# Kernel optimization log

Hardware: AMD Instinct MI355X
Metric: run time of the kernel (lower is better)

The kernel has to match this reference:

```python
import jax, jax.numpy as jnp
import numpy as np

K = 7        # neighborhood kernel size
HEADS = 4


def _layernorm(x, g, b, eps=1e-5):
    m = x.mean(-1, keepdims=True)
    v = x.var(-1, keepdims=True)
    return (x - m) * jax.lax.rsqrt(v + eps) * g + b


def _neigh_idx(n, k):
    # NATTEN semantics: window of size k centered on the query, shifted to stay in-bounds.
    starts = np.clip(np.arange(n) - k // 2, 0, n - k)
    idx = starts[:, None] + np.arange(k)                 # (n, k) absolute neighbor coords
    rel = idx - np.arange(n)[:, None] + (k - 1)          # (n, k) in [0, 2k-2] -> rpb index
    return jnp.asarray(idx), jnp.asarray(rel)


def _na2d(x, qkv_w, qkv_b, rpb, proj_w, proj_b, k=K, heads=HEADS):
    # x: (B, H, W, C) neighborhood attention (NATTEN NeighborhoodAttention2D)
    B, H, W, C = x.shape
    dh = C // heads
    qkv = (x @ qkv_w + qkv_b).reshape(B, H, W, 3, heads, dh)
    q = qkv[..., 0, :, :] * (dh ** -0.5)                 # (B,H,W,n,d)
    kk = qkv[..., 1, :, :]
    v = qkv[..., 2, :, :]
    ih, rh = _neigh_idx(H, k)
    iw, rw = _neigh_idx(W, k)
    kg = kk[:, ih][:, :, :, iw]                          # (B,H,k,W,k,n,d)
    vg = v[:, ih][:, :, :, iw]
    logits = jnp.einsum('bhwnd,bhiwjnd->bnhwij', q, kg)  # (B,n,H,W,k,k)
    bias = rpb[:, rh][:, :, :, rw]                       # (n,H,k,W,k)
    bias = jnp.transpose(bias, (0, 1, 3, 2, 4))          # (n,H,W,k,k)
    logits = logits + bias[None]
    attn = jax.nn.softmax(logits.reshape(B, heads, H, W, k * k), axis=-1)
    attn = attn.reshape(B, heads, H, W, k, k)
    out = jnp.einsum('bnhwij,bhiwjnd->bhwnd', attn, vg).reshape(B, H, W, C)
    return out @ proj_w + proj_b


def _mixffn(x, fc1_w, fc1_b, dw_w, dw_b, fc2_w, fc2_b, b, t, H, W):
    # PosFeedForward3d: fc1 -> depthwise Conv3d(3x3x3) over (T,H,W) -> GELU -> fc2
    h = x @ fc1_w + fc1_b                                # (b*t, H*W, M)
    M = h.shape[-1]
    h = h.reshape(b, t, H, W, M)
    h = jax.lax.conv_general_dilated(
        h, dw_w, window_strides=(1, 1, 1), padding='SAME',
        dimension_numbers=('NDHWC', 'DHWIO', 'NDHWC'), feature_group_count=M) + dw_b
    h = jax.nn.gelu(h, approximate=False)
    h = h.reshape(b * t, H * W, M)
    return h @ fc2_w + fc2_b


def setup_inputs() -> dict:
    key = jax.random.key(0)
    B, C, T, H, W = 2, 128, 8, 40, 40
    L, M, k, n = 2, 512, K, HEADS
    ks = jax.random.split(key, 12)
    s = 0.02
    return {
        'x': jax.random.normal(ks[0], (B, C, T, H, W), jnp.float32),
        'ln1_g': jnp.ones((L, C)), 'ln1_b': jnp.zeros((L, C)),
        'qkv_w': jax.random.normal(ks[1], (L, C, 3 * C), jnp.float32) * s,
        'qkv_b': jnp.zeros((L, 3 * C)),
        'rpb': jax.random.normal(ks[2], (L, n, 2 * k - 1, 2 * k - 1), jnp.float32) * s,
        'proj_w': jax.random.normal(ks[3], (L, C, C), jnp.float32) * s,
        'proj_b': jnp.zeros((L, C)),
        'ln2_g': jnp.ones((L, C)), 'ln2_b': jnp.zeros((L, C)),
        'fc1_w': jax.random.normal(ks[4], (L, C, M), jnp.float32) * s,
        'fc1_b': jnp.zeros((L, M)),
        'dw_w': jax.random.normal(ks[5], (L, 3, 3, 3, 1, M), jnp.float32) * s,
        'dw_b': jnp.zeros((L, M)),
        'fc2_w': jax.random.normal(ks[6], (L, M, C), jnp.float32) * s,
        'fc2_b': jnp.zeros((L, C)),
        'out_g': jnp.ones((C,)), 'out_b': jnp.zeros((C,)),
    }


def reference(x, ln1_g, ln1_b, qkv_w, qkv_b, rpb, proj_w, proj_b,
              ln2_g, ln2_b, fc1_w, fc1_b, dw_w, dw_b, fc2_w, fc2_b, out_g, out_b):
    b, c, t, H, W = x.shape
    h = jnp.transpose(x, (0, 2, 3, 4, 1)).reshape(b * t, H, W, c)
    L = qkv_w.shape[0]
    for i in range(L):
        h = _na2d(_layernorm(h, ln1_g[i], ln1_b[i]), qkv_w[i], qkv_b[i], rpb[i], proj_w[i], proj_b[i]) + h
        h2 = h.reshape(b * t, H * W, c)
        h2 = _mixffn(_layernorm(h2, ln2_g[i], ln2_b[i]), fc1_w[i], fc1_b[i], dw_w[i], dw_b[i], fc2_w[i], fc2_b[i], b, t, H, W) + h2
        h = h2.reshape(b * t, H, W, c)
    h = _layernorm(h, out_g, out_b)
    return jnp.transpose(h.reshape(b, t, H, W, c), (0, 4, 1, 2, 3))
```

## Files before the change

### kernel.cpp

```cpp
#include <hip/hip_runtime.h>
#include <hip/hip_bf16.h>
#include <math.h>

typedef __hip_bfloat16 bf16;
typedef __attribute__((ext_vector_type(8))) short short8;
typedef __attribute__((ext_vector_type(4))) float floatx4;
typedef __attribute__((ext_vector_type(2))) float f32x2;
typedef _Float16 h2 __attribute__((ext_vector_type(2)));
typedef __fp16 hraw2 __attribute__((ext_vector_type(2)));

static __device__ __forceinline__ h2 cvt2h(float a, float b) {
    union { hraw2 r; h2 h; } u;
    u.r = __builtin_amdgcn_cvt_pkrtz(a, b);
    return u.h;
}

#define HH 40
#define WW 40
#define CC 128
#define TT 8
#define NIMG 16
#define NTOK 25600
#define MDIM 512
#define NHEAD 4
#define KVP 1608
#define VP  1280
#define LGS 60

#define WT_QKV 0
#define WT_PROJ 49152
#define WT_FC1  65536
#define WT_FC2  131072
#define WT_L    196608

__global__ __launch_bounds__(256) void k_transpose_in(const float* __restrict__ x,
                                                      float* __restrict__ h) {
    int blk = blockIdx.x;
    int n = blk / 200; int r = blk % 200; int ci = r / 50, ri = r % 50;
    int b = n >> 3, t = n & 7;
    int c0 = ci * 32, r0 = ri * 32;
    __shared__ float tile[32][33];
    int tid = threadIdx.x;
    int lc = tid >> 5, lr = tid & 31;
    #pragma unroll
    for (int it = 0; it < 4; ++it) {
        int cc = it * 8 + lc;
        tile[cc][lr] = x[((size_t)((b * 128 + c0 + cc) * 8 + t)) * 1600 + r0 + lr];
    }
    __syncthreads();
    #pragma unroll
    for (int it = 0; it < 4; ++it) {
        int rr = it * 8 + lc;
        h[((size_t)(n * 1600 + r0 + rr)) * 128 + c0 + lr] = tile[lr][rr];
    }
}

__global__ __launch_bounds__(256) void k_wt(const float* __restrict__ qkv_w,
                                            const float* __restrict__ proj_w,
                                            const float* __restrict__ fc1_w,
                                            const float* __restrict__ fc2_w,
                                            bf16* __restrict__ wt) {
    __shared__ float tile[64][65];
    int id = blockIdx.x;
    int l = id / 48, r = id % 48;
    const float* src; bf16* dst; int K_, N_, t;
    if (r < 12)      { src = qkv_w  + l * 128 * 384; dst = wt + l * WT_L + WT_QKV; K_ = 128; N_ = 384; t = r; }
    else if (r < 16) { src = proj_w + l * 128 * 128; dst = wt + l * WT_L + WT_PROJ; K_ = 128; N_ = 128; t = r - 12; }
    else if (r < 32) { src = fc1_w  + l * 128 * 512; dst = wt + l * WT_L + WT_FC1; K_ = 128; N_ = 512; t = r - 16; }
    else             { src = fc2_w  + l * 512 * 128; dst = wt + l * WT_L + WT_FC2; K_ = 512; N_ = 128; t = r - 32; }
    int KT = K_ >> 6;
    int k0 = (t % KT) * 64, n0 = (t / KT) * 64;
    int tid = threadIdx.x;
    for (int c = tid; c < 4096; c += 256) {
        int kk = c >> 6, nn = c & 63;
        tile[kk][nn] = src[(size_t)(k0 + kk) * N_ + n0 + nn];
    }
    __syncthreads();
    for (int c = tid; c < 4096; c += 256) {
        int nn = c >> 6, kk = c & 63;
        dst[(size_t)(n0 + nn) * K_ + k0 + kk] = __float2bfloat16(tile[kk][nn]);
    }
}

template<typename OutT>
__global__ __launch_bounds__(256) void k_lngemm(const float* __restrict__ A,
                                                const bf16* __restrict__ Bt,
                                                const float* __restrict__ g,
                                                const float* __restrict__ be,
                                                const float* __restrict__ bias,
                                                OutT* __restrict__ D,
                                                int N) {
    constexpr int LDK = 40;
    __shared__ bf16 As[64 * LDK];
    __shared__ bf16 Bs[128 * LDK];
    __shared__ float sMean[64], sRstd[64], sG[128], sB[128];
    int tid = threadIdx.x;
    int m0 = blockIdx.y * 64, n0 = blockIdx.x * 128;
    {
        int row = tid >> 2, q4 = tid & 3;
        const float* p = A + (size_t)(m0 + row) * 128 + q4 * 32;
        float s = 0.f, q = 0.f;
        #pragma unroll
        for (int i = 0; i < 32; i += 4) {
            float4 f = *(const float4*)(p + i);
            s += f.x + f.y + f.z + f.w;
            q += f.x * f.x + f.y * f.y + f.z * f.z + f.w * f.w;
        }
        s += __shfl_xor(s, 1); q += __shfl_xor(q, 1);
        s += __shfl_xor(s, 2); q += __shfl_xor(q, 2);
        if (q4 == 0) {
            float mean = s * (1.0f / 128.0f);
            float var = q * (1.0f / 128.0f) - mean * mean;
            sMean[row] = mean;
            sRstd[row] = rsqrtf(var + 1e-5f);
        }
        if (tid < 128) { sG[tid] = g[tid]; sB[tid] = be[tid]; }
    }
    __syncthreads();
    int wave = tid >> 6, lane = tid & 63;
    int l15 = lane & 15, quad = lane >> 4;
    int wr = wave >> 1, wc = wave & 1;
    floatx4 acc[2][4];
    #pragma unroll
    for (int i = 0; i < 2; ++i)
        #pragma unroll
        for (int j = 0; j < 4; ++j)
            acc[i][j] = (floatx4){0.f, 0.f, 0.f, 0.f};

    for (int k0 = 0; k0 < 128; k0 += 32) {
        #pragma unroll
        for (int it = 0; it < 2; ++it) {
            int c = tid + it * 256;
            int row = c >> 3, kq = (c & 7) * 4;
            float4 f = *(const float4*)(A + (size_t)(m0 + row) * 128 + k0 + kq);
            float mean = sMean[row], rst = sRstd[row];
            float r0v = (f.x - mean) * rst * sG[k0 + kq]     + sB[k0 + kq];
            float r1v = (f.y - mean) * rst * sG[k0 + kq + 1] + sB[k0 + kq + 1];
            float r2v = (f.z - mean) * rst * sG[k0 + kq + 2] + sB[k0 + kq + 2];
            float r3v = (f.w - mean) * rst * sG[k0 + kq + 3] + sB[k0 + kq + 3];
            __hip_bfloat162 p0, p1;
            p0.x = __float2bfloat16(r0v); p0.y = __float2bfloat16(r1v);
            p1.x = __float2bfloat16(r2v); p1.y = __float2bfloat16(r3v);
            *(__hip_bfloat162*)&As[row * LDK + kq]     = p0;
            *(__hip_bfloat162*)&As[row * LDK + kq + 2] = p1;
        }
        #pragma unroll
        for (int c = tid; c < 512; c += 256) {
            int row = c >> 2, off = (c & 3) * 8;
            *(uint4*)&Bs[row * LDK + off] =
                *(const uint4*)&Bt[(size_t)(n0 + row) * 128 + k0 + off];
        }
        __syncthreads();
        short8 af[2], bfr[4];
        #pragma unroll
        for (int i = 0; i < 2; ++i)
            af[i] = *(const short8*)&As[(wr * 32 + i * 16 + l15) * LDK + quad * 8];
        #pragma unroll
        for (int j = 0; j < 4; ++j)
            bfr[j] = *(const short8*)&Bs[(wc * 64 + j * 16 + l15) * LDK + quad * 8];
        #pragma unroll
        for (int i = 0; i < 2; ++i)
            #pragma unroll
            for (int j = 0; j < 4; ++j)
                acc[i][j] = __builtin_amdgcn_mfma_f32_16x16x32_bf16(af[i], bfr[j], acc[i][j], 0, 0, 0);
        __syncthreads();
    }
    #pragma unroll
    for (int i = 0; i < 2; ++i) {
        #pragma unroll
        for (int j = 0; j < 4; ++j) {
            int nn = n0 + wc * 64 + j * 16 + l15;
            float bv = bias[nn];
            #pragma unroll
            for (int rg = 0; rg < 4; ++rg) {
                int m = m0 + wr * 32 + i * 16 + quad * 4 + rg;
                float v = acc[i][j][rg] + bv;
                if constexpr (sizeof(OutT) == 2)
                    D[(size_t)m * N + nn] = __float2bfloat16(v);
                else
                    D[(size_t)m * N + nn] = v;
            }
        }
    }
}

template<int BM, int BN, int WM, int WN, typename OutT>
__global__ __launch_bounds__(256) void k_gemm_mfma(const bf16* __restrict__ A,
                                                   const bf16* __restrict__ Bt,
                                                   const float* __restrict__ bias,
                                                   const float* __restrict__ R,
                                                   OutT* __restrict__ D,
                                                   int K, int N) {
    constexpr int LDK = 40;
    __shared__ bf16 As[BM * LDK];
    __shared__ bf16 Bs[BN * LDK];
    int tid = threadIdx.x;
    int wave = tid >> 6, lane = tid & 63;
    int l15 = lane & 15, quad = lane >> 4;
    constexpr int WCOLS = BN / WN;
    int wr = wave / WCOLS, wc = wave % WCOLS;
    int m0 = blockIdx.y * BM, n0 = blockIdx.x * BN;
    constexpr int MI = WM / 16, NJ = WN / 16;
    floatx4 acc[MI][NJ];
    #pragma unroll
    for (int i = 0; i < MI; ++i)
        #pragma unroll
        for (int j = 0; j < NJ; ++j)
            acc[i][j] = (floatx4){0.f, 0.f, 0.f, 0.f};

    for (int k0 = 0; k0 < K; k0 += 32) {
        #pragma unroll
        for (int c = tid; c < BM * 4; c += 256) {
            int row = c >> 2, off = (c & 3) * 8;
            *(uint4*)&As[row * LDK + off] =
                *(const uint4*)&A[(size_t)(m0 + row) * K + k0 + off];
        }
        #pragma unroll
        for (int c = tid; c < BN * 4; c += 256) {
            int row = c >> 2, off = (c & 3) * 8;
            *(uint4*)&Bs[row * LDK + off] =
                *(const uint4*)&Bt[(size_t)(n0 + row) * K + k0 + off];
        }
        __syncthreads();
        short8 af[MI], bfr[NJ];
        #pragma unroll
        for (int i = 0; i < MI; ++i)
            af[i] = *(const short8*)&As[(wr * WM + i * 16 + l15) * LDK + quad * 8];
        #pragma unroll
        for (int j = 0; j < NJ; ++j)
            bfr[j] = *(const short8*)&Bs[(wc * WN + j * 16 + l15) * LDK + quad * 8];
        #pragma unroll
        for (int i = 0; i < MI; ++i)
            #pragma unroll
            for (int j = 0; j < NJ; ++j)
                acc[i][j] = __builtin_amdgcn_mfma_f32_16x16x32_bf16(af[i], bfr[j], acc[i][j], 0, 0, 0);
        __syncthreads();
    }
    #pragma unroll
    for (int i = 0; i < MI; ++i) {
        #pragma unroll
        for (int j = 0; j < NJ; ++j) {
            int nn = n0 + wc * WN + j * 16 + l15;
            float bv = bias[nn];
            #pragma unroll
            for (int rg = 0; rg < 4; ++rg) {
                int m = m0 + wr * WM + i * 16 + quad * 4 + rg;
                float v = acc[i][j][rg] + bv;
                if (R) v += R[(size_t)m * N + nn];
                if constexpr (sizeof(OutT) == 2)
                    D[(size_t)m * N + nn] = __float2bfloat16(v);
                else
                    D[(size_t)m * N + nn] = v;
            }
        }
    }
}

__global__ __launch_bounds__(256) void k_gemm_ln(const bf16* __restrict__ A,
                                                 const bf16* __restrict__ Bt,
                                                 const float* __restrict__ bias,
                                                 const float* __restrict__ R,
                                                 const float* __restrict__ g,
                                                 const float* __restrict__ be,
                                                 float* __restrict__ Dres,
                                                 bf16* __restrict__ Aout,
                                                 int K) {
    constexpr int LDK = 40;
    __shared__ bf16 As[32 * LDK];
    __shared__ bf16 Bs[128 * LDK];
    __shared__ float pSum[2][32], pSq[2][32];
    __shared__ float sG[128], sB[128];
    int tid = threadIdx.x;
    int wave = tid >> 6, lane = tid & 63;
    int l15 = lane & 15, quad = lane >> 4;
    int wr = wave >> 1, wc = wave & 1;
    int m0 = blockIdx.x * 32;
    if (tid < 128) { sG[tid] = g[tid]; sB[tid] = be[tid]; }
    floatx4 acc[4];
    #pragma unroll
    for (int j = 0; j < 4; ++j) acc[j] = (floatx4){0.f, 0.f, 0.f, 0.f};

    for (int k0 = 0; k0 < K; k0 += 32) {
        if (tid < 128) {
            int row = tid >> 2, off = (tid & 3) * 8;
            *(uint4*)&As[row * LDK + off] =
                *(const uint4*)&A[(size_t)(m0 + row) * K + k0 + off];
        }
        #pragma unroll
        for (int c = tid; c < 512; c += 256) {
            int row = c >> 2, off = (c & 3) * 8;
            *(uint4*)&Bs[row * LDK + off] =
                *(const uint4*)&Bt[(size_t)row * K + k0 + off];
        }
        __syncthreads();
        short8 af = *(const short8*)&As[(wr * 16 + l15) * LDK + quad * 8];
        short8 bfr[4];
        #pragma unroll
        for (int j = 0; j < 4; ++j)
            bfr[j] = *(const short8*)&Bs[(wc * 64 + j * 16 + l15) * LDK + quad * 8];
        #pragma unroll
        for (int j = 0; j < 4; ++j)
            acc[j] = __builtin_amdgcn_mfma_f32_16x16x32_bf16(af, bfr[j], acc[j], 0, 0, 0);
        __syncthreads();
    }
    float v[4][4];
    float s[4] = {0.f, 0.f, 0.f, 0.f};
    float q[4] = {0.f, 0.f, 0.f, 0.f};
    #pragma unroll
    for (int j = 0; j < 4; ++j) {
        int nn = wc * 64 + j * 16 + l15;
        float bv = bias[nn];
        #pragma unroll
        for (int rg = 0; rg < 4; ++rg) {
            int m = wr * 16 + quad * 4 + rg;
            float val = acc[j][rg] + bv + R[(size_t)(m0 + m) * 128 + nn];
            v[j][rg] = val;
            s[rg] += val; q[rg] += val * val;
        }
    }
    #pragma unroll
    for (int o = 8; o > 0; o >>= 1) {
        #pragma unroll
        for (int rg = 0; rg < 4; ++rg) {
            s[rg] += __shfl_xor(s[rg], o);
            q[rg] += __shfl_xor(q[rg], o);
        }
    }
    if (l15 == 0) {
        #pragma unroll
        for (int rg = 0; rg < 4; ++rg) {
            int row = wr * 16 + quad * 4 + rg;
            pSum[wc][row] = s[rg];
            pSq[wc][row]  = q[rg];
        }
    }
    __syncthreads();
    #pragma unroll
    for (int rg = 0; rg < 4; ++rg) {
        int row = wr * 16 + quad * 4 + rg;
        float tot = pSum[0][row] + pSum[1][row];
        float tq  = pSq[0][row]  + pSq[1][row];
        float mean = tot * (1.0f / 128.0f);
        float var = tq * (1.0f / 128.0f) - mean * mean;
        float rst = rsqrtf(var + 1e-5f);
        size_t rb = (size_t)(m0 + row) * 128;
        #pragma unroll
        for (int j = 0; j < 4; ++j) {
            int nn = wc * 64 + j * 16 + l15;
            Dres[rb + nn] = v[j][rg];
            Aout[rb + nn] = __float2bfloat16((v[j][rg] - mean) * rst * sG[nn] + sB[nn]);
        }
    }
}

__global__ __launch_bounds__(256) void k_gemm_lnout(const bf16* __restrict__ A,
                                                    const bf16* __restrict__ Bt,
                                                    const float* __restrict__ bias,
                                                    const float* __restrict__ R,
                                                    const float* __restrict__ g,
                                                    const float* __restrict__ be,
                                                    float* __restrict__ out,
                                                    int K) {
    constexpr int LDK = 40;
    __shared__ bf16 As[32 * LDK];
    __shared__ bf16 Bs[128 * LDK];
    __shared__ float ot[32][133];
    __shared__ float sG[128], sB[128];
    int tid = threadIdx.x;
    int wave = tid >> 6, lane = tid & 63;
    int l15 = lane & 15, quad = lane >> 4;
    int wr = wave >> 1, wc = wave & 1;
    int m0 = blockIdx.x * 32;
    if (tid < 128) { sG[tid] = g[tid]; sB[tid] = be[tid]; }
    floatx4 acc[4];
    #pragma unroll
    for (int j = 0; j < 4; ++j) acc[j] = (floatx4){0.f, 0.f, 0.f, 0.f};

    for (int k0 = 0; k0 < K; k0 += 32) {
        if (tid < 128) {
            int row = tid >> 2, off = (tid & 3) * 8;
            *(uint4*)&As[row * LDK + off] =
                *(const uint4*)&A[(size_t)(m0 + row) * K + k0 + off];
        }
        #pragma unroll
        for (int c = tid; c < 512; c += 256) {
            int row = c >> 2, off = (c & 3) * 8;
            *(uint4*)&Bs[row * LDK + off] =
                *(const uint4*)&Bt[(size_t)row * K + k0 + off];
        }
        __syncthreads();
        short8 af = *(const short8*)&As[(wr * 16 + l15) * LDK + quad * 8];
        short8 bfr[4];
        #pragma unroll
        for (int j = 0; j < 4; ++j)
            bfr[j] = *(const short8*)&Bs[(wc * 64 + j * 16 + l15) * LDK + quad * 8];
        #pragma unroll
        for (int j = 0; j < 4; ++j)
            acc[j] = __builtin_amdgcn_mfma_f32_16x16x32_bf16(af, bfr[j], acc[j], 0, 0, 0);
        __syncthreads();
    }
    #pragma unroll
    for (int j = 0; j < 4; ++j) {
        int nn = wc * 64 + j * 16 + l15;
        float bv = bias[nn];
        #pragma unroll
        for (int rg = 0; rg < 4; ++rg) {
            int m = wr * 16 + quad * 4 + rg;
            ot[m][nn] = acc[j][rg] + bv + R[(size_t)(m0 + m) * 128 + nn];
        }
    }
    __syncthreads();
    int row = tid >> 3, sub = tid & 7;
    float vv[16];
    float s = 0.f, q = 0.f;
    #pragma unroll
    for (int i = 0; i < 16; ++i) {
        float v = ot[row][sub * 16 + i];
        vv[i] = v; s += v; q += v * v;
    }
    #pragma unroll
    for (int o = 4; o > 0; o >>= 1) { s += __shfl_xor(s, o); q += __shfl_xor(q, o); }
    float mean = s * (1.0f / 128.0f);
    float var = q * (1.0f / 128.0f) - mean * mean;
    float rst = rsqrtf(var + 1e-5f);
    #pragma unroll
    for (int i = 0; i < 16; ++i) {
        int ch = sub * 16 + i;
        ot[row][ch] = (vv[i] - mean) * rst * sG[ch] + sB[ch];
    }
    __syncthreads();
    int n = m0 / 1600, rem0 = m0 % 1600;
    int b = n >> 3, t = n & 7;
    #pragma unroll
    for (int it = 0; it < 16; ++it) {
        int idx = it * 256 + tid;
        int ch = idx >> 5, tk = idx & 31;
        out[((size_t)((b * 128 + ch) * 8 + t)) * 1600 + rem0 + tk] = ot[tk][ch];
    }
}

__global__ __launch_bounds__(256) void k_attn(const bf16* __restrict__ qkv,
                                              const float* __restrict__ rpb,
                                              bf16* __restrict__ out) {
    int raw = blockIdx.x;
    int blk = (raw & 7) * 320 + (raw >> 3);
    int head = blk & 3;
    int ny = blk >> 2;
    int n = ny / 40, y = ny % 40;
    int sy = min(max(y - 3, 0), HH - 7);
    __shared__ __align__(16) short KVs[7 * KVP];
    __shared__ __align__(16) float lg[40][LGS];
    int tid = threadIdx.x;
    for (int i2 = tid; i2 < 1120; i2 += 256) {
        int d8 = i2 & 3, kx = (i2 >> 2) % 40, ky = i2 / 160;
        size_t base = ((size_t)(n * 1600 + (sy + ky) * 40 + kx)) * 384 + 128 + head * 32 + d8 * 8;
        union { uint4 u; __hip_bfloat162 b[4]; } U;
        U.u = *(const uint4*)(qkv + base);
        union { short8 s; h2 h[4]; } W;
        #pragma unroll
        for (int c = 0; c < 4; ++c) {
            float2 f = __bfloat1622float2(U.b[c]);
            W.h[c] = cvt2h(f.x, f.y);
        }
        *(short8*)&KVs[ky * KVP + kx * 40 + d8 * 8] = W.s;
    }
    __syncthreads();
    for (int p2 = tid; p2 < 280; p2 += 256) {
        int xq = p2 / 7, ky = p2 - (p2 / 7) * 7;
        int sx = min(max(xq - 3, 0), WW - 7);
        const bf16* qg = qkv + ((size_t)(n * 1600 + y * 40 + xq)) * 384 + head * 32;
        union { uint4 u; __hip_bfloat162 b[4]; } U[4];
        #pragma unroll
        for (int u = 0; u < 4; ++u) U[u].u = *(const uint4*)(qg + u * 8);
        h2 qh[16];
        #pragma unroll
        for (int c = 0; c < 16; ++c) {
            float2 f = __bfloat1622float2(U[c >> 2].b[c & 3]);
            qh[c] = cvt2h(f.x, f.y);
        }
        const float* rb = rpb + head * 169 + (sy + ky - y + 6) * 13 + (sx - xq + 6);
        int kbase = ky * KVP + sx * 40;
        #pragma unroll
        for (int jx = 0; jx < 7; ++jx) {
            const h2* kp = (const h2*)&KVs[kbase + jx * 40];
            float dot = 0.f;
            #pragma unroll
            for (int c = 0; c < 16; ++c)
                dot = __builtin_amdgcn_fdot2(qh[c], kp[c], dot, false);
            lg[xq][ky * 8 + jx] = dot * 0.1767766952966369f + rb[jx];
        }
        lg[xq][ky * 8 + 7] = -1e30f;
    }
    __syncthreads();
    for (int i2 = tid; i2 < 1120; i2 += 256) {
        int d8 = i2 & 3, kx = (i2 >> 2) % 40, ky = i2 / 160;
        size_t base = ((size_t)(n * 1600 + (sy + ky) * 40 + kx)) * 384 + 256 + head * 32 + d8 * 8;
        *(uint4*)&KVs[ky * VP + kx * 32 + d8 * 8] = *(const uint4*)(qkv + base);
    }
    if (tid < 160) {
        int row = tid >> 2, q = tid & 3;
        int nb = (q == 3) ? 2 : 4;
        const float4* lp = (const float4*)&lg[row][q * 16];
        float4 f[4];
        #pragma unroll
        for (int i = 0; i < 4; ++i)
            if (i < nb) f[i] = lp[i];
        float m = -1e30f;
        #pragma unroll
        for (int i = 0; i < 4; ++i)
            if (i < nb) m = fmaxf(m, fmaxf(fmaxf(f[i].x, f[i].y), fmaxf(f[i].z, f[i].w)));
        m = fmaxf(m, __shfl_xor(m, 1));
        m = fmaxf(m, __shfl_xor(m, 2));
        float s = 0.f;
        #pragma unroll
        for (int i = 0; i < 4; ++i)
            if (i < nb) {
                f[i].x = expf(f[i].x - m); f[i].y = expf(f[i].y - m);
                f[i].z = expf(f[i].z - m); f[i].w = expf(f[i].w - m);
                s += f[i].x + f[i].y + f[i].z + f[i].w;
            }
        s += __shfl_xor(s, 1);
        s += __shfl_xor(s, 2);
        float inv = 1.0f / s;
        float4* sp = (float4*)&lg[row][q * 16];
        #pragma unroll
        for (int i = 0; i < 4; ++i)
            if (i < nb) {
                f[i].x *= inv; f[i].y *= inv; f[i].z *= inv; f[i].w *= inv;
                sp[i] = f[i];
            }
    }
    __syncthreads();
    for (int o = tid; o < 320; o += 256) {
        int xq = o >> 3, cq = o & 7;
        int sx = min(max(xq - 3, 0), WW - 7);
        float a0 = 0.f, a1 = 0.f, a2 = 0.f, a3 = 0.f;
        #pragma unroll
        for (int ky = 0; ky < 7; ++ky) {
            float4 pa = *(const float4*)&lg[xq][ky * 8];
            float4 pb = *(const float4*)&lg[xq][ky * 8 + 4];
            float ps[8] = {pa.x, pa.y, pa.z, pa.w, pb.x, pb.y, pb.z, pb.w};
            int vb = ky * VP + sx * 32 + cq * 4;
            #pragma unroll
            for (int jx = 0; jx < 7; ++jx) {
                float p = ps[jx];
                uint2 vv = *(const uint2*)&KVs[vb + jx * 32];
                float2 v0 = __bfloat1622float2(*(const __hip_bfloat162*)&vv.x);
                float2 v1 = __bfloat1622float2(*(const __hip_bfloat162*)&vv.y);
                a0 += p * v0.x; a1 += p * v0.y;
                a2 += p * v1.x; a3 += p * v1.y;
            }
        }
        __hip_bfloat162 o01, o23;
        o01.x = __float2bfloat16(a0); o01.y = __float2bfloat16(a1);
        o23.x = __float2bfloat16(a2); o23.y = __float2bfloat16(a3);
        bf16* op = out + ((size_t)(n * 1600 + y * 40 + xq)) * 128 + head * 32 + cq * 4;
        *(__hip_bfloat162*)op = o01;
        *(__hip_bfloat162*)(op + 2) = o23;
    }
}

template<int X0>
__device__ __forceinline__ void dw_body(const float* __restrict__ inp,
                                        const int* roff, const float* wr,
                                        float bs, int m, size_t outbase,
                                        bf16* __restrict__ outp) {
    float c0[9], c1[9], c2[9];
    #pragma unroll
    for (int p = 0; p < 9; ++p) {
        c0[p] = (X0 > 0) ? inp[roff[p] + (X0 - 1) * 512 + m] : 0.f;
        c1[p] = inp[roff[p] + X0 * 512 + m];
        c2[p] = inp[roff[p] + (X0 + 1) * 512 + m];
    }
    #pragma unroll
    for (int xi = 0; xi < 20; ++xi) {
        constexpr int XN_BASE = X0 + 2;
        int x = X0 + xi;
        float cn[9];
        if (XN_BASE + xi < 40) {
            #pragma unroll
            for (int p = 0; p < 9; ++p)
                cn[p] = inp[roff[p] + (XN_BASE + xi) * 512 + m];
        } else {
            #pragma unroll
            for (int p = 0; p < 9; ++p) cn[p] = 0.f;
        }
        float acc = bs;
        #pragma unroll
        for (int p = 0; p < 9; ++p)
            acc += wr[p * 3 + 0] * c0[p] + wr[p * 3 + 1] * c1[p] + wr[p * 3 + 2] * c2[p];
        float g = 0.5f * acc * (1.0f + erff(acc * 0.70710678118654752f));
        outp[outbase + (size_t)x * 512] = __float2bfloat16(g);
        #pragma unroll
        for (int p = 0; p < 9; ++p) { c0[p] = c1[p]; c1[p] = c2[p]; c2[p] = cn[p]; }
    }
}

__global__ __launch_bounds__(512, 4) void k_dwconv(const float* __restrict__ inp,
                                                   const float* __restrict__ w,
                                                   const float* __restrict__ bias,
                                                   bf16* __restrict__ outp) {
    int raw = blockIdx.x;
    int blk = (raw & 7) * 160 + (raw >> 3);
    int xh = blk & 1;
    int ny = blk >> 1;
    int n = ny / 40, y = ny - n * 40;
    int b = n >> 3, t = n & 7;
    int m = threadIdx.x;
    float wr[27];
    int roff[9];
    #pragma unroll
    for (int dt = 0; dt < 3; ++dt) {
        #pragma unroll
        for (int dy = 0; dy < 3; ++dy) {
            int p = dt * 3 + dy;
            int tt = t + dt - 1, yy = y + dy - 1;
            bool v = (tt >= 0 && tt < 8 && yy >= 0 && yy < 40);
            int tc = min(max(tt, 0), 7), yc = min(max(yy, 0), 39);
            roff[p] = ((b * 8 + tc) * 1600 + yc * 40) * 512;
            #pragma unroll
            for (int q = 0; q < 3; ++q)
                wr[p * 3 + q] = v ? w[(p * 3 + q) * 512 + m] : 0.f;
        }
    }
    float bs = bias[m];
    size_t outbase = ((size_t)(n * 1600 + y * 40)) * 512 + m;
    if (xh == 0)
        dw_body<0>(inp, roff, wr, bs, m, outbase, outp);
    else
        dw_body<20>(inp, roff, wr, bs, m, outbase, outp);
}

extern "C" void kernel_launch(void* const* d_in, const int* in_sizes, int n_in,
                              void* d_out, int out_size, void* d_ws, size_t ws_size,
                              hipStream_t stream) {
    const float* x      = (const float*)d_in[0];
    const float* ln1_g  = (const float*)d_in[1];
    const float* ln1_b  = (const float*)d_in[2];
    const float* qkv_w  = (const float*)d_in[3];
    const float* qkv_b  = (const float*)d_in[4];
    const float* rpb    = (const float*)d_in[5];
    const float* proj_w = (const float*)d_in[6];
    const float* proj_b = (const float*)d_in[7];
    const float* ln2_g  = (const float*)d_in[8];
    const float* ln2_b  = (const float*)d_in[9];
    const float* fc1_w  = (const float*)d_in[10];
    const float* fc1_b  = (const float*)d_in[11];
    const float* dw_w   = (const float*)d_in[12];
    const float* dw_b   = (const float*)d_in[13];
    const float* fc2_w  = (const float*)d_in[14];
    const float* fc2_b  = (const float*)d_in[15];
    const float* out_g  = (const float*)d_in[16];
    const float* out_b  = (const float*)d_in[17];
    float* out = (float*)d_out;

    float* h     = (float*)d_ws;
    float* f1    = h + (size_t)NTOK * 128;
    bf16* qkvb   = (bf16*)(f1 + (size_t)NTOK * 512);
    bf16* f2b    = qkvb + (size_t)NTOK * 384;
    bf16* abufA  = f2b  + (size_t)NTOK * 512;
    bf16* abufL  = abufA + (size_t)NTOK * 128;
    bf16* wt     = abufL + (size_t)NTOK * 128;

    k_wt<<<96, 256, 0, stream>>>(qkv_w, proj_w, fc1_w, fc2_w, wt);
    k_transpose_in<<<NIMG * 200, 256, 0, stream>>>(x, h);
    for (int l = 0; l < 2; ++l) {
        const bf16* wtl = wt + (size_t)l * WT_L;
        if (l == 0) {
            k_lngemm<bf16><<<dim3(3, 400), 256, 0, stream>>>(
                h, wtl + WT_QKV, ln1_g, ln1_b, qkv_b, qkvb, 384);
        } else {
            k_gemm_mfma<64, 128, 32, 64, bf16><<<dim3(3, 400), 256, 0, stream>>>(
                abufL, wtl + WT_QKV, qkv_b + 384, nullptr, qkvb, 128, 384);
        }
        k_attn<<<NIMG * HH * NHEAD, 256, 0, stream>>>(qkvb, rpb + l * 4 * 169, abufA);
        k_gemm_ln<<<800, 256, 0, stream>>>(
            abufA, wtl + WT_PROJ, proj_b + l * 128, h,
            ln2_g + l * 128, ln2_b + l * 128, h, abufL, 128);
        k_gemm_mfma<64, 128, 32, 64, float><<<dim3(4, 400), 256, 0, stream>>>(
            abufL, wtl + WT_FC1, fc1_b + l * 512, nullptr, f1, 128, 512);
        k_dwconv<<<NIMG * HH * 2, 512, 0, stream>>>(f1, dw_w + l * 27 * 512, dw_b + l * 512, f2b);
        if (l == 0) {
            k_gemm_ln<<<800, 256, 0, stream>>>(
                f2b, wtl + WT_FC2, fc2_b, h,
                ln1_g + 128, ln1_b + 128, h, abufL, 512);
        } else {
            k_gemm_lnout<<<800, 256, 0, stream>>>(
                f2b, wtl + WT_FC2, fc2_b + 128, h, out_g, out_b, out, 512);
        }
    }
}
```

Baseline: 365.1 us.

## Store fc1 output in bf16, merge prep kernels, widen attention blocks to 320 threads

```diff
diff --git a/kernel.cpp b/kernel.cpp
--- a/kernel.cpp
+++ b/kernel.cpp
@@ -33,52 +33,51 @@
 #define WT_FC2  131072
 #define WT_L    196608
 
-__global__ __launch_bounds__(256) void k_transpose_in(const float* __restrict__ x,
-                                                      float* __restrict__ h) {
-    int blk = blockIdx.x;
-    int n = blk / 200; int r = blk % 200; int ci = r / 50, ri = r % 50;
-    int b = n >> 3, t = n & 7;
-    int c0 = ci * 32, r0 = ri * 32;
-    __shared__ float tile[32][33];
+__global__ __launch_bounds__(256) void k_prep(const float* __restrict__ x,
+                                              const float* __restrict__ qkv_w,
+                                              const float* __restrict__ proj_w,
+                                              const float* __restrict__ fc1_w,
+                                              const float* __restrict__ fc2_w,
+                                              float* __restrict__ h,
+                                              bf16* __restrict__ wt) {
+    __shared__ float tileU[64 * 65];
     int tid = threadIdx.x;
-    int lc = tid >> 5, lr = tid & 31;
-    #pragma unroll
-    for (int it = 0; it < 4; ++it) {
-        int cc = it * 8 + lc;
-        tile[cc][lr] = x[((size_t)((b * 128 + c0 + cc) * 8 + t)) * 1600 + r0 + lr];
-    }
-    __syncthreads();
-    #pragma unroll
-    for (int it = 0; it < 4; ++it) {
-        int rr = it * 8 + lc;
-        h[((size_t)(n * 1600 + r0 + rr)) * 128 + c0 + lr] = tile[lr][rr];
-    }
-}
-
-__global__ __launch_bounds__(256) void k_wt(const float* __restrict__ qkv_w,
-                                            const float* __restrict__ proj_w,
-                                            const float* __restrict__ fc1_w,
-                                            const float* __restrict__ fc2_w,
-                                            bf16* __restrict__ wt) {
-    __shared__ float tile[64][65];
-    int id = blockIdx.x;
-    int l = id / 48, r = id % 48;
-    const float* src; bf16* dst; int K_, N_, t;
-    if (r < 12)      { src = qkv_w  + l * 128 * 384; dst = wt + l * WT_L + WT_QKV; K_ = 128; N_ = 384; t = r; }
-    else if (r < 16) { src = proj_w + l * 128 * 128; dst = wt + l * WT_L + WT_PROJ; K_ = 128; N_ = 128; t = r - 12; }
-    else if (r < 32) { src = fc1_w  + l * 128 * 512; dst = wt + l * WT_L + WT_FC1; K_ = 128; N_ = 512; t = r - 16; }
-    else             { src = fc2_w  + l * 512 * 128; dst = wt + l * WT_L + WT_FC2; K_ = 512; N_ = 128; t = r - 32; }
-    int KT = K_ >> 6;
-    int k0 = (t % KT) * 64, n0 = (t / KT) * 64;
-    int tid = threadIdx.x;
-    for (int c = tid; c < 4096; c += 256) {
-        int kk = c >> 6, nn = c & 63;
-        tile[kk][nn] = src[(size_t)(k0 + kk) * N_ + n0 + nn];
-    }
-    __syncthreads();
-    for (int c = tid; c < 4096; c += 256) {
-        int nn = c >> 6, kk = c & 63;
-        dst[(size_t)(n0 + nn) * K_ + k0 + kk] = __float2bfloat16(tile[kk][nn]);
+    if (blockIdx.x < 96) {
+        int id = blockIdx.x;
+        int l = id / 48, r = id % 48;
+        const float* src; bf16* dst; int K_, N_, t;
+        if (r < 12)      { src = qkv_w  + l * 128 * 384; dst = wt + l * WT_L + WT_QKV; K_ = 128; N_ = 384; t = r; }
+        else if (r < 16) { src = proj_w + l * 128 * 128; dst = wt + l * WT_L + WT_PROJ; K_ = 128; N_ = 128; t = r - 12; }
+        else if (r < 32) { src = fc1_w  + l * 128 * 512; dst = wt + l * WT_L + WT_FC1; K_ = 128; N_ = 512; t = r - 16; }
+        else             { src = fc2_w  + l * 512 * 128; dst = wt + l * WT_L + WT_FC2; K_ = 512; N_ = 128; t = r - 32; }
+        int KT = K_ >> 6;
+        int k0 = (t % KT) * 64, n0 = (t / KT) * 64;
+        for (int c = tid; c < 4096; c += 256) {
+            int kk = c >> 6, nn = c & 63;
+            tileU[kk * 65 + nn] = src[(size_t)(k0 + kk) * N_ + n0 + nn];
+        }
+        __syncthreads();
+        for (int c = tid; c < 4096; c += 256) {
+            int nn = c >> 6, kk = c & 63;
+            dst[(size_t)(n0 + nn) * K_ + k0 + kk] = __float2bfloat16(tileU[kk * 65 + nn]);
+        }
+    } else {
+        int blk = blockIdx.x - 96;
+        int n = blk / 200; int r = blk % 200; int ci = r / 50, ri = r % 50;
+        int b = n >> 3, t = n & 7;
+        int c0 = ci * 32, r0 = ri * 32;
+        int lc = tid >> 5, lr = tid & 31;
+        #pragma unroll
+        for (int it = 0; it < 4; ++it) {
+            int cc = it * 8 + lc;
+            tileU[cc * 33 + lr] = x[((size_t)((b * 128 + c0 + cc) * 8 + t)) * 1600 + r0 + lr];
+        }
+        __syncthreads();
+        #pragma unroll
+        for (int it = 0; it < 4; ++it) {
+            int rr = it * 8 + lc;
+            h[((size_t)(n * 1600 + r0 + rr)) * 128 + c0 + lr] = tileU[lr * 33 + rr];
+        }
     }
 }
 
@@ -439,7 +438,7 @@
     }
 }
 
-__global__ __launch_bounds__(256) void k_attn(const bf16* __restrict__ qkv,
+__global__ __launch_bounds__(320) void k_attn(const bf16* __restrict__ qkv,
                                               const float* __restrict__ rpb,
                                               bf16* __restrict__ out) {
     int raw = blockIdx.x;
@@ -451,7 +450,7 @@
     __shared__ __align__(16) short KVs[7 * KVP];
     __shared__ __align__(16) float lg[40][LGS];
     int tid = threadIdx.x;
-    for (int i2 = tid; i2 < 1120; i2 += 256) {
+    for (int i2 = tid; i2 < 1120; i2 += 320) {
         int d8 = i2 & 3, kx = (i2 >> 2) % 40, ky = i2 / 160;
         size_t base = ((size_t)(n * 1600 + (sy + ky) * 40 + kx)) * 384 + 128 + head * 32 + d8 * 8;
         union { uint4 u; __hip_bfloat162 b[4]; } U;
@@ -465,8 +464,8 @@
         *(short8*)&KVs[ky * KVP + kx * 40 + d8 * 8] = W.s;
     }
     __syncthreads();
-    for (int p2 = tid; p2 < 280; p2 += 256) {
-        int xq = p2 / 7, ky = p2 - (p2 / 7) * 7;
+    if (tid < 280) {
+        int xq = tid / 7, ky = tid - (tid / 7) * 7;
         int sx = min(max(xq - 3, 0), WW - 7);
         const bf16* qg = qkv + ((size_t)(n * 1600 + y * 40 + xq)) * 384 + head * 32;
         union { uint4 u; __hip_bfloat162 b[4]; } U[4];
@@ -492,7 +491,7 @@
         lg[xq][ky * 8 + 7] = -1e30f;
     }
     __syncthreads();
-    for (int i2 = tid; i2 < 1120; i2 += 256) {
+    for (int i2 = tid; i2 < 1120; i2 += 320) {
         int d8 = i2 & 3, kx = (i2 >> 2) % 40, ky = i2 / 160;
         size_t base = ((size_t)(n * 1600 + (sy + ky) * 40 + kx)) * 384 + 256 + head * 32 + d8 * 8;
         *(uint4*)&KVs[ky * VP + kx * 32 + d8 * 8] = *(const uint4*)(qkv + base);
@@ -531,8 +530,8 @@
             }
     }
     __syncthreads();
-    for (int o = tid; o < 320; o += 256) {
-        int xq = o >> 3, cq = o & 7;
+    {
+        int xq = tid >> 3, cq = tid & 7;
         int sx = min(max(xq - 3, 0), WW - 7);
         float a0 = 0.f, a1 = 0.f, a2 = 0.f, a3 = 0.f;
         #pragma unroll
@@ -561,16 +560,16 @@
 }
 
 template<int X0>
-__device__ __forceinline__ void dw_body(const float* __restrict__ inp,
+__device__ __forceinline__ void dw_body(const bf16* __restrict__ inp,
                                         const int* roff, const float* wr,
                                         float bs, int m, size_t outbase,
                                         bf16* __restrict__ outp) {
     float c0[9], c1[9], c2[9];
     #pragma unroll
     for (int p = 0; p < 9; ++p) {
-        c0[p] = (X0 > 0) ? inp[roff[p] + (X0 - 1) * 512 + m] : 0.f;
-        c1[p] = inp[roff[p] + X0 * 512 + m];
-        c2[p] = inp[roff[p] + (X0 + 1) * 512 + m];
+        c0[p] = (X0 > 0) ? __bfloat162float(inp[roff[p] + (X0 - 1) * 512 + m]) : 0.f;
+        c1[p] = __bfloat162float(inp[roff[p] + X0 * 512 + m]);
+        c2[p] = __bfloat162float(inp[roff[p] + (X0 + 1) * 512 + m]);
     }
     #pragma unroll
     for (int xi = 0; xi < 20; ++xi) {
@@ -580,7 +579,7 @@
         if (XN_BASE + xi < 40) {
             #pragma unroll
             for (int p = 0; p < 9; ++p)
-                cn[p] = inp[roff[p] + (XN_BASE + xi) * 512 + m];
+                cn[p] = __bfloat162float(inp[roff[p] + (XN_BASE + xi) * 512 + m]);
         } else {
             #pragma unroll
             for (int p = 0; p < 9; ++p) cn[p] = 0.f;
@@ -596,7 +595,7 @@
     }
 }
 
-__global__ __launch_bounds__(512, 4) void k_dwconv(const float* __restrict__ inp,
+__global__ __launch_bounds__(512, 4) void k_dwconv(const bf16* __restrict__ inp,
                                                    const float* __restrict__ w,
                                                    const float* __restrict__ bias,
                                                    bf16* __restrict__ outp) {
@@ -655,15 +654,14 @@
     float* out = (float*)d_out;
 
     float* h     = (float*)d_ws;
-    float* f1    = h + (size_t)NTOK * 128;
-    bf16* qkvb   = (bf16*)(f1 + (size_t)NTOK * 512);
+    bf16* f1b    = (bf16*)(h + (size_t)NTOK * 128);
+    bf16* qkvb   = f1b  + (size_t)NTOK * 512;
     bf16* f2b    = qkvb + (size_t)NTOK * 384;
     bf16* abufA  = f2b  + (size_t)NTOK * 512;
     bf16* abufL  = abufA + (size_t)NTOK * 128;
     bf16* wt     = abufL + (size_t)NTOK * 128;
 
-    k_wt<<<96, 256, 0, stream>>>(qkv_w, proj_w, fc1_w, fc2_w, wt);
-    k_transpose_in<<<NIMG * 200, 256, 0, stream>>>(x, h);
+    k_prep<<<96 + NIMG * 200, 256, 0, stream>>>(x, qkv_w, proj_w, fc1_w, fc2_w, h, wt);
     for (int l = 0; l < 2; ++l) {
         const bf16* wtl = wt + (size_t)l * WT_L;
         if (l == 0) {
@@ -673,13 +671,13 @@
             k_gemm_mfma<64, 128, 32, 64, bf16><<<dim3(3, 400), 256, 0, stream>>>(
                 abufL, wtl + WT_QKV, qkv_b + 384, nullptr, qkvb, 128, 384);
         }
-        k_attn<<<NIMG * HH * NHEAD, 256, 0, stream>>>(qkvb, rpb + l * 4 * 169, abufA);
+        k_attn<<<NIMG * HH * NHEAD, 320, 0, stream>>>(qkvb, rpb + l * 4 * 169, abufA);
         k_gemm_ln<<<800, 256, 0, stream>>>(
             abufA, wtl + WT_PROJ, proj_b + l * 128, h,
             ln2_g + l * 128, ln2_b + l * 128, h, abufL, 128);
-        k_gemm_mfma<64, 128, 32, 64, float><<<dim3(4, 400), 256, 0, stream>>>(
-            abufL, wtl + WT_FC1, fc1_b + l * 512, nullptr, f1, 128, 512);
-        k_dwconv<<<NIMG * HH * 2, 512, 0, stream>>>(f1, dw_w + l * 27 * 512, dw_b + l * 512, f2b);
+        k_gemm_mfma<64, 128, 32, 64, bf16><<<dim3(4, 400), 256, 0, stream>>>(
+            abufL, wtl + WT_FC1, fc1_b + l * 512, nullptr, f1b, 128, 512);
+        k_dwconv<<<NIMG * HH * 2, 512, 0, stream>>>(f1b, dw_w + l * 27 * 512, dw_b + l * 512, f2b);
         if (l == 0) {
             k_gemm_ln<<<800, 256, 0, stream>>>(
                 f2b, wtl + WT_FC2, fc2_b, h,
```

New measurement: 338.8 us, median of 2. 1.08x faster.
